# Kernel optimization log

Hardware: AMD Instinct MI355X
Metric: run time of the kernel (lower is better)

The kernel has to match this reference:

```python
import jax, jax.numpy as jnp
import numpy as np

NUM_HEADS = 12
HEAD_DIM = 64
SCALE = HEAD_DIM ** -0.5


def setup_inputs() -> dict:
    key = jax.random.key(0)
    ks = jax.random.split(key, 5)
    B, N, C = 8, 1024, 768
    x = jax.random.normal(ks[0], (B, N, C), dtype=jnp.float32)
    qkv_w = jax.random.normal(ks[1], (3 * C, C), dtype=jnp.float32) * (C ** -0.5)
    qkv_b = jax.random.normal(ks[2], (3 * C,), dtype=jnp.float32) * 0.02
    proj_w = jax.random.normal(ks[3], (C, C), dtype=jnp.float32) * (C ** -0.5)
    proj_b = jax.random.normal(ks[4], (C,), dtype=jnp.float32) * 0.02
    return {"x": x, "qkv_w": qkv_w, "qkv_b": qkv_b, "proj_w": proj_w, "proj_b": proj_b}


def reference(x, qkv_w, qkv_b, proj_w, proj_b):
    B, N, C = x.shape
    H, D = NUM_HEADS, HEAD_DIM
    # qkv projection: (B,N,3C) -> (3,B,H,N,D)
    qkv = (x @ qkv_w.T + qkv_b).reshape(B, N, 3, H, D).transpose(2, 0, 3, 1, 4)
    q, k, v = qkv[0], qkv[1], qkv[2]
    q = q * SCALE
    # full N x N attention scores, softmax over keys
    attn = jax.nn.softmax(jnp.einsum("bhnd,bhmd->bhnm", q, k), axis=-1)
    # Libragrad: detach the softmax map before multiplying with V
    attn = jax.lax.stop_gradient(attn)
    out = jnp.einsum("bhnm,bhmd->bhnd", attn, v)  # (B,H,N,D)
    out = out.transpose(0, 2, 1, 3).reshape(B, N, C)
    return out @ proj_w.T + proj_b
```

## Files before the change

### kernel.cpp

```cpp
#include <hip/hip_runtime.h>

#define NH 12
#define HD 64
#define BB 8
#define SEQ 1024
#define CD 768

typedef __bf16 bf16x8 __attribute__((ext_vector_type(8)));
typedef float f32x4 __attribute__((ext_vector_type(4)));

__device__ __forceinline__ unsigned short f2bf(float f) {
    unsigned int u = __float_as_uint(f);
    u = (u + 0x7fffu + ((u >> 16) & 1u)) >> 16;
    return (unsigned short)u;
}

__device__ __forceinline__ void gld_lds16(const unsigned short* g, unsigned short* l) {
    __builtin_amdgcn_global_load_lds(
        (const __attribute__((address_space(1))) unsigned int*)g,
        (__attribute__((address_space(3))) unsigned int*)l, 16, 0, 0);
}

__device__ __forceinline__ int slot2key(int s) {
    return (s & 3) + 4 * ((s >> 3) & 3) + 16 * ((s >> 2) & 1) + 32 * (s >> 5);
}

#define N4_X 1572864
#define N4_W1 442368
#define N4_W2 147456
__global__ void cast_all(const float* __restrict__ x, const float* __restrict__ w1,
                         const float* __restrict__ w2,
                         unsigned short* __restrict__ ox, unsigned short* __restrict__ ow1,
                         unsigned short* __restrict__ ow2) {
    int i = blockIdx.x * blockDim.x + threadIdx.x;
    const float4* src;
    ushort4* dst;
    if (i < N4_X) {
        src = (const float4*)x + i; dst = (ushort4*)ox + i;
    } else if (i < N4_X + N4_W1) {
        src = (const float4*)w1 + (i - N4_X); dst = (ushort4*)ow1 + (i - N4_X);
    } else if (i < N4_X + N4_W1 + N4_W2) {
        src = (const float4*)w2 + (i - N4_X - N4_W1); dst = (ushort4*)ow2 + (i - N4_X - N4_W1);
    } else return;
    float4 f = *src;
    ushort4 o;
    o.x = f2bf(f.x); o.y = f2bf(f.y); o.z = f2bf(f.z); o.w = f2bf(f.w);
    *dst = o;
}

template<int MODE>
__global__ __launch_bounds__(256)
void gemm_bt(const unsigned short* __restrict__ A, const unsigned short* __restrict__ W,
             const float* __restrict__ bias,
             unsigned short* __restrict__ qb, unsigned short* __restrict__ kb,
             unsigned short* __restrict__ vb, float* __restrict__ fout,
             int M, int N, int K) {
    __shared__ __attribute__((aligned(16))) unsigned short As[2][128 * 32];
    __shared__ __attribute__((aligned(16))) unsigned short Bs[2][128 * 32];

    const int t    = threadIdx.x;
    const int bm0  = blockIdx.x * 128;
    const int bn0  = blockIdx.y * 128;
    const int wave = t >> 6;
    const int lane = t & 63;
    const int wm   = (wave >> 1) * 64;
    const int wn   = (wave & 1) * 64;
    const int col  = lane & 15;
    const int quad = lane >> 4;

    const int srow = t >> 2;
    const int scol = (t & 3) * 8;

    f32x4 acc[4][4];
#pragma unroll
    for (int i = 0; i < 4; i++)
#pragma unroll
        for (int j = 0; j < 4; j++) acc[i][j] = (f32x4){0.f, 0.f, 0.f, 0.f};

    auto stage = [&](int it, unsigned short* Ad, unsigned short* Bd) {
        const int k0 = it << 5;
        gld_lds16(A + (size_t)(bm0 + srow) * K + k0 + scol,      Ad + srow * 32 + scol);
        gld_lds16(A + (size_t)(bm0 + 64 + srow) * K + k0 + scol, Ad + (64 + srow) * 32 + scol);
        gld_lds16(W + (size_t)(bn0 + srow) * K + k0 + scol,      Bd + srow * 32 + scol);
        gld_lds16(W + (size_t)(bn0 + 64 + srow) * K + k0 + scol, Bd + (64 + srow) * 32 + scol);
    };
    auto compute = [&](const unsigned short* Ad, const unsigned short* Bd) {
        bf16x8 af[4], bf[4];
#pragma unroll
        for (int mi = 0; mi < 4; mi++)
            af[mi] = *(const bf16x8*)(Ad + (wm + mi * 16 + col) * 32 + quad * 8);
#pragma unroll
        for (int ni = 0; ni < 4; ni++)
            bf[ni] = *(const bf16x8*)(Bd + (wn + ni * 16 + col) * 32 + quad * 8);
#pragma unroll
        for (int mi = 0; mi < 4; mi++)
#pragma unroll
            for (int ni = 0; ni < 4; ni++)
                acc[mi][ni] = __builtin_amdgcn_mfma_f32_16x16x32_bf16(
                    af[mi], bf[ni], acc[mi][ni], 0, 0, 0);
    };

    const int nIt = K >> 5;
    stage(0, As[0], Bs[0]);
#pragma unroll 1
    for (int it = 0; it < nIt; it += 2) {
        __syncthreads();
        if (it + 1 < nIt) stage(it + 1, As[1], Bs[1]);
        compute(As[0], Bs[0]);
        __syncthreads();
        if (it + 2 < nIt) stage(it + 2, As[0], Bs[0]);
        compute(As[1], Bs[1]);
    }

    if (MODE == 1) {
#pragma unroll
        for (int mi = 0; mi < 4; mi++)
#pragma unroll
            for (int ni = 0; ni < 4; ni++) {
                const int n = bn0 + wn + ni * 16 + col;
                const float bv = bias[n];
#pragma unroll
                for (int r = 0; r < 4; r++) {
                    const int m = bm0 + wm + mi * 16 + quad * 4 + r;
                    fout[(size_t)m * N + n] = acc[mi][ni][r] + bv;
                }
            }
        return;
    }

    const int sel = bn0 / 768;
    const int nb  = bn0 - sel * 768;
    const int b   = bm0 >> 10;
    const int nqb = bm0 & 1023;
    unsigned short* const dstbuf = (sel == 0) ? qb : (sel == 1) ? kb : vb;
    const float scale = (sel == 0) ? 0.18033688f : 1.0f;

#pragma unroll
    for (int ni = 0; ni < 4; ni++) {
        const int hn = nb + wn + ni * 16;
        const int h  = hn >> 6;
        const int d0 = hn & 63;
        const float bv = bias[bn0 + wn + ni * 16 + col];
        unsigned short* const rowbase =
            dstbuf + ((size_t)(b * NH + h) * SEQ) * HD + d0 + col;
#pragma unroll
        for (int mi = 0; mi < 4; mi++)
#pragma unroll
            for (int r = 0; r < 4; r++) {
                const int nq = nqb + wm + mi * 16 + quad * 4 + r;
                rowbase[(size_t)nq * HD] = f2bf((acc[mi][ni][r] + bv) * scale);
            }
    }
}

__global__ __launch_bounds__(256)
void vtrans(const unsigned short* __restrict__ v, unsigned short* __restrict__ vt) {
    __shared__ __attribute__((aligned(16))) unsigned short T[64 * 72];
    const int bh = blockIdx.x;
    const int kt = blockIdx.y;
    const int t  = threadIdx.x;
    const int r  = t >> 2;
    const int c  = (t & 3) * 16;

    const unsigned short* src = v + ((size_t)bh * SEQ + kt * 64 + r) * HD + c;
    *(uint4*)(T + r * 72 + c)     = *(const uint4*)src;
    *(uint4*)(T + r * 72 + c + 8) = *(const uint4*)(src + 8);
    __syncthreads();

    union { unsigned short us[16]; uint4 u4[2]; } o;
#pragma unroll
    for (int j = 0; j < 16; j++) o.us[j] = T[slot2key(c + j) * 72 + r];
    unsigned short* dst = vt + ((size_t)bh * HD + r) * SEQ + kt * 64 + c;
    *(uint4*)dst       = o.u4[0];
    *(uint4*)(dst + 8) = o.u4[1];
}

__global__ __launch_bounds__(256, 4)
void attn_mfma(const unsigned short* __restrict__ qb,
               const unsigned short* __restrict__ kb,
               const unsigned short* __restrict__ vb,
               unsigned short* __restrict__ ob) {
    __shared__ __attribute__((aligned(16))) unsigned short Ks[2][64 * 72];
    __shared__ __attribute__((aligned(16))) unsigned short VT[2][64 * 72];

    const int t  = threadIdx.x;
    const int bh = blockIdx.x;
    const int qt = blockIdx.y;
    const size_t base = (size_t)bh * SEQ * HD;

    const int sr = t >> 2;
    const int sc = (t & 3) * 16;

    const int wave = t >> 6;
    const int lane = t & 63;
    const int col  = lane & 15;
    const int quad = lane >> 4;

    bf16x8 aq0, aq1;
    {
        const int q = qt * 64 + wave * 16 + col;
        aq0 = *(const bf16x8*)(qb + base + (size_t)q * HD + quad * 8);
        aq1 = *(const bf16x8*)(qb + base + (size_t)q * HD + 32 + quad * 8);
    }

    float l_r = 0.f;
    f32x4 accO[4];
#pragma unroll
    for (int di = 0; di < 4; di++) accO[di] = (f32x4){0.f, 0.f, 0.f, 0.f};

    const unsigned short* kp = kb + base + (size_t)sr * HD + sc;
    const unsigned short* vp = vb + base + (size_t)sr * SEQ + sc;
    const int so = sr * 72 + sc;

    uint4 kr0 = *(const uint4*)kp,  kr1 = *(const uint4*)(kp + 8);
    uint4 vr0 = *(const uint4*)vp,  vr1 = *(const uint4*)(vp + 8);
    *(uint4*)(Ks[0] + so)     = kr0;
    *(uint4*)(Ks[0] + so + 8) = kr1;
    *(uint4*)(VT[0] + so)     = vr0;
    *(uint4*)(VT[0] + so + 8) = vr1;
    kr0 = *(const uint4*)(kp + 64 * HD);  kr1 = *(const uint4*)(kp + 64 * HD + 8);
    vr0 = *(const uint4*)(vp + 64);       vr1 = *(const uint4*)(vp + 64 + 8);

    auto chunk = [&](int kc, const unsigned short* Kc, const unsigned short* Vc,
                     unsigned short* Kn, unsigned short* Vn) {
        __syncthreads();
        if (kc < 15) {
            *(uint4*)(Kn + so)     = kr0;
            *(uint4*)(Kn + so + 8) = kr1;
            *(uint4*)(Vn + so)     = vr0;
            *(uint4*)(Vn + so + 8) = vr1;
        }
        if (kc < 14) {
            const unsigned short* kn = kp + (size_t)(kc + 2) * 64 * HD;
            const unsigned short* vn = vp + (size_t)(kc + 2) * 64;
            kr0 = *(const uint4*)kn; kr1 = *(const uint4*)(kn + 8);
            vr0 = *(const uint4*)vn; vr1 = *(const uint4*)(vn + 8);
        }

        f32x4 accT[4];
        __builtin_amdgcn_s_setprio(1);
#pragma unroll
        for (int ni = 0; ni < 4; ni++) {
            bf16x8 bk0 = *(const bf16x8*)(Kc + (ni * 16 + col) * 72 + quad * 8);
            bf16x8 bk1 = *(const bf16x8*)(Kc + (ni * 16 + col) * 72 + 32 + quad * 8);
            f32x4 z = (f32x4){0.f, 0.f, 0.f, 0.f};
            z = __builtin_amdgcn_mfma_f32_16x16x32_bf16(bk0, aq0, z, 0, 0, 0);
            z = __builtin_amdgcn_mfma_f32_16x16x32_bf16(bk1, aq1, z, 0, 0, 0);
            accT[ni] = z;
        }
        __builtin_amdgcn_s_setprio(0);

        union { __bf16 b[16]; bf16x8 v[2]; } apu;
#pragma unroll
        for (int ni = 0; ni < 4; ni++) {
            float p0 = __builtin_exp2f(accT[ni][0]);
            float p1 = __builtin_exp2f(accT[ni][1]);
            float p2 = __builtin_exp2f(accT[ni][2]);
            float p3 = __builtin_exp2f(accT[ni][3]);
            l_r += (p0 + p1) + (p2 + p3);
            apu.b[ni * 4 + 0] = (__bf16)p0;
            apu.b[ni * 4 + 1] = (__bf16)p1;
            apu.b[ni * 4 + 2] = (__bf16)p2;
            apu.b[ni * 4 + 3] = (__bf16)p3;
        }

        __builtin_amdgcn_s_setprio(1);
#pragma unroll
        for (int di = 0; di < 4; di++) {
            bf16x8 bv0 = *(const bf16x8*)(Vc + (di * 16 + col) * 72 + quad * 8);
            bf16x8 bv1 = *(const bf16x8*)(Vc + (di * 16 + col) * 72 + 32 + quad * 8);
            accO[di] = __builtin_amdgcn_mfma_f32_16x16x32_bf16(apu.v[0], bv0, accO[di], 0, 0, 0);
            accO[di] = __builtin_amdgcn_mfma_f32_16x16x32_bf16(apu.v[1], bv1, accO[di], 0, 0, 0);
        }
        __builtin_amdgcn_s_setprio(0);
    };

#pragma unroll 1
    for (int kc2 = 0; kc2 < 16; kc2 += 2) {
        chunk(kc2,     Ks[0], VT[0], Ks[1], VT[1]);
        chunk(kc2 + 1, Ks[1], VT[1], Ks[0], VT[0]);
    }

    const int b = bh / NH, h = bh - b * NH;
    float s = l_r;
    s += __shfl_xor(s, 16);
    s += __shfl_xor(s, 32);
#pragma unroll
    for (int r = 0; r < 4; r++) {
        const float inv = 1.f / __shfl(s, quad * 4 + r);
        const int q = qt * 64 + wave * 16 + quad * 4 + r;
        const size_t rowbase = ((size_t)b * SEQ + q) * CD + h * 64;
#pragma unroll
        for (int di = 0; di < 4; di++)
            ob[rowbase + di * 16 + col] = f2bf(accO[di][r] * inv);
    }
}

extern "C" void kernel_launch(void* const* d_in, const int* in_sizes, int n_in,
                              void* d_out, int out_size, void* d_ws, size_t ws_size,
                              hipStream_t stream) {
    const float* x      = (const float*)d_in[0];
    const float* qkv_w  = (const float*)d_in[1];
    const float* qkv_b  = (const float*)d_in[2];
    const float* proj_w = (const float*)d_in[3];
    const float* proj_b = (const float*)d_in[4];
    float* out = (float*)d_out;

    char* ws = (char*)d_ws;
    unsigned short* x_bf     = (unsigned short*)ws;
    unsigned short* qkvw_bf  = (unsigned short*)(ws + 12582912);
    unsigned short* projw_bf = (unsigned short*)(ws + 12582912 + 3538944);
    unsigned short* q_bf     = (unsigned short*)(ws + 12582912 + 3538944 + 1179648);
    unsigned short* k_bf     = q_bf + 6291456;
    unsigned short* v_bf     = k_bf + 6291456;
    unsigned short* vt_bf    = x_bf;
    unsigned short* attn_bf  = v_bf;

    cast_all<<<8448, 256, 0, stream>>>(x, qkv_w, proj_w, x_bf, qkvw_bf, projw_bf);

    gemm_bt<0><<<dim3(64, 18), 256, 0, stream>>>(x_bf, qkvw_bf, qkv_b,
                                                 q_bf, k_bf, v_bf, nullptr,
                                                 8192, 2304, 768);

    vtrans<<<dim3(96, 16), 256, 0, stream>>>(v_bf, vt_bf);

    attn_mfma<<<dim3(96, 16), 256, 0, stream>>>(q_bf, k_bf, vt_bf, attn_bf);

    gemm_bt<1><<<dim3(64, 6), 256, 0, stream>>>(attn_bf, projw_bf, proj_b,
                                                nullptr, nullptr, nullptr, out,
                                                8192, 768, 768);
}
```

Baseline: 198.4 us.

## Fuse fp32-to-bf16 cast of x into QKV GEMM A-tile loading

The separate pass that cast x to bf16 is removed. The QKV GEMM now loads fp32 A tiles into registers two iterations ahead, converts them to bf16 and writes them to LDS after each compute step. This drops a full write and re-read of the bf16 copy of x and shrinks the cast kernel to weights only. In exchange the GEMM reads twice as many bytes for A, uses more registers for prefetch, and A loads no longer go directly to LDS, which may hurt occupancy or overlap. Rounding now comes from the compiler's __bf16 conversion instead of the manual routine.

```diff
diff --git a/kernel.cpp b/kernel.cpp
--- a/kernel.cpp
+++ b/kernel.cpp
@@ -25,22 +25,17 @@
     return (s & 3) + 4 * ((s >> 3) & 3) + 16 * ((s >> 2) & 1) + 32 * (s >> 5);
 }
 
-#define N4_X 1572864
 #define N4_W1 442368
 #define N4_W2 147456
-__global__ void cast_all(const float* __restrict__ x, const float* __restrict__ w1,
-                         const float* __restrict__ w2,
-                         unsigned short* __restrict__ ox, unsigned short* __restrict__ ow1,
-                         unsigned short* __restrict__ ow2) {
+__global__ void cast_all(const float* __restrict__ w1, const float* __restrict__ w2,
+                         unsigned short* __restrict__ ow1, unsigned short* __restrict__ ow2) {
     int i = blockIdx.x * blockDim.x + threadIdx.x;
     const float4* src;
     ushort4* dst;
-    if (i < N4_X) {
-        src = (const float4*)x + i; dst = (ushort4*)ox + i;
-    } else if (i < N4_X + N4_W1) {
-        src = (const float4*)w1 + (i - N4_X); dst = (ushort4*)ow1 + (i - N4_X);
-    } else if (i < N4_X + N4_W1 + N4_W2) {
-        src = (const float4*)w2 + (i - N4_X - N4_W1); dst = (ushort4*)ow2 + (i - N4_X - N4_W1);
+    if (i < N4_W1) {
+        src = (const float4*)w1 + i; dst = (ushort4*)ow1 + i;
+    } else if (i < N4_W1 + N4_W2) {
+        src = (const float4*)w2 + (i - N4_W1); dst = (ushort4*)ow2 + (i - N4_W1);
     } else return;
     float4 f = *src;
     ushort4 o;
@@ -50,7 +45,8 @@
 
 template<int MODE>
 __global__ __launch_bounds__(256)
-void gemm_bt(const unsigned short* __restrict__ A, const unsigned short* __restrict__ W,
+void gemm_bt(const float* __restrict__ Af, const unsigned short* __restrict__ Ab,
+             const unsigned short* __restrict__ W,
              const float* __restrict__ bias,
              unsigned short* __restrict__ qb, unsigned short* __restrict__ kb,
              unsigned short* __restrict__ vb, float* __restrict__ fout,
@@ -77,12 +73,35 @@
 #pragma unroll
         for (int j = 0; j < 4; j++) acc[i][j] = (f32x4){0.f, 0.f, 0.f, 0.f};
 
-    auto stage = [&](int it, unsigned short* Ad, unsigned short* Bd) {
+    auto stageB = [&](int it, unsigned short* Bd) {
         const int k0 = it << 5;
-        gld_lds16(A + (size_t)(bm0 + srow) * K + k0 + scol,      Ad + srow * 32 + scol);
-        gld_lds16(A + (size_t)(bm0 + 64 + srow) * K + k0 + scol, Ad + (64 + srow) * 32 + scol);
         gld_lds16(W + (size_t)(bn0 + srow) * K + k0 + scol,      Bd + srow * 32 + scol);
         gld_lds16(W + (size_t)(bn0 + 64 + srow) * K + k0 + scol, Bd + (64 + srow) * 32 + scol);
+    };
+    auto stageAb = [&](int it, unsigned short* Ad) {
+        const int k0 = it << 5;
+        gld_lds16(Ab + (size_t)(bm0 + srow) * K + k0 + scol,      Ad + srow * 32 + scol);
+        gld_lds16(Ab + (size_t)(bm0 + 64 + srow) * K + k0 + scol, Ad + (64 + srow) * 32 + scol);
+    };
+    auto loadA = [&](int it, float4 (&r)[4]) {
+        const int k0 = it << 5;
+        const float* p0 = Af + (size_t)(bm0 + srow) * K + k0 + scol;
+        const float* p1 = Af + (size_t)(bm0 + 64 + srow) * K + k0 + scol;
+        r[0] = *(const float4*)p0; r[1] = *(const float4*)(p0 + 4);
+        r[2] = *(const float4*)p1; r[3] = *(const float4*)(p1 + 4);
+    };
+    auto writeA = [&](const float4 (&r)[4], unsigned short* Ad) {
+        union { __bf16 b[8]; uint4 u; } w0, w1;
+        w0.b[0] = (__bf16)r[0].x; w0.b[1] = (__bf16)r[0].y;
+        w0.b[2] = (__bf16)r[0].z; w0.b[3] = (__bf16)r[0].w;
+        w0.b[4] = (__bf16)r[1].x; w0.b[5] = (__bf16)r[1].y;
+        w0.b[6] = (__bf16)r[1].z; w0.b[7] = (__bf16)r[1].w;
+        w1.b[0] = (__bf16)r[2].x; w1.b[1] = (__bf16)r[2].y;
+        w1.b[2] = (__bf16)r[2].z; w1.b[3] = (__bf16)r[2].w;
+        w1.b[4] = (__bf16)r[3].x; w1.b[5] = (__bf16)r[3].y;
+        w1.b[6] = (__bf16)r[3].z; w1.b[7] = (__bf16)r[3].w;
+        *(uint4*)(Ad + srow * 32 + scol)        = w0.u;
+        *(uint4*)(Ad + (64 + srow) * 32 + scol) = w1.u;
     };
     auto compute = [&](const unsigned short* Ad, const unsigned short* Bd) {
         bf16x8 af[4], bf[4];
@@ -101,15 +120,39 @@
     };
 
     const int nIt = K >> 5;
-    stage(0, As[0], Bs[0]);
+    float4 ra0[4], ra1[4];
+    if constexpr (MODE == 0) {
+        loadA(0, ra0); writeA(ra0, As[0]);
+        loadA(1, ra1);
+        stageB(0, Bs[0]);
+    } else {
+        stageAb(0, As[0]);
+        stageB(0, Bs[0]);
+    }
 #pragma unroll 1
     for (int it = 0; it < nIt; it += 2) {
         __syncthreads();
-        if (it + 1 < nIt) stage(it + 1, As[1], Bs[1]);
+        if (it + 1 < nIt) stageB(it + 1, Bs[1]);
+        if constexpr (MODE == 0) {
+            if (it + 2 < nIt) loadA(it + 2, ra0);
+        } else {
+            if (it + 1 < nIt) stageAb(it + 1, As[1]);
+        }
         compute(As[0], Bs[0]);
+        if constexpr (MODE == 0) {
+            if (it + 1 < nIt) writeA(ra1, As[1]);
+        }
         __syncthreads();
-        if (it + 2 < nIt) stage(it + 2, As[0], Bs[0]);
+        if (it + 2 < nIt) stageB(it + 2, Bs[0]);
+        if constexpr (MODE == 0) {
+            if (it + 3 < nIt) loadA(it + 3, ra1);
+        } else {
+            if (it + 2 < nIt) stageAb(it + 2, As[0]);
+        }
         compute(As[1], Bs[1]);
+        if constexpr (MODE == 0) {
+            if (it + 2 < nIt) writeA(ra0, As[0]);
+        }
     }
 
     if (MODE == 1) {
@@ -316,9 +359,9 @@
     unsigned short* vt_bf    = x_bf;
     unsigned short* attn_bf  = v_bf;
 
-    cast_all<<<8448, 256, 0, stream>>>(x, qkv_w, proj_w, x_bf, qkvw_bf, projw_bf);
-
-    gemm_bt<0><<<dim3(64, 18), 256, 0, stream>>>(x_bf, qkvw_bf, qkv_b,
+    cast_all<<<2304, 256, 0, stream>>>(qkv_w, proj_w, qkvw_bf, projw_bf);
+
+    gemm_bt<0><<<dim3(64, 18), 256, 0, stream>>>(x, nullptr, qkvw_bf, qkv_b,
                                                  q_bf, k_bf, v_bf, nullptr,
                                                  8192, 2304, 768);
 
@@ -326,7 +369,7 @@
 
     attn_mfma<<<dim3(96, 16), 256, 0, stream>>>(q_bf, k_bf, vt_bf, attn_bf);
 
-    gemm_bt<1><<<dim3(64, 6), 256, 0, stream>>>(attn_bf, projw_bf, proj_b,
+    gemm_bt<1><<<dim3(64, 6), 256, 0, stream>>>(nullptr, attn_bf, projw_bf, proj_b,
                                                 nullptr, nullptr, nullptr, out,
                                                 8192, 768, 768);
 }
```

Measured after the change: 217.4 us. 1.1x slower.

## Process two query sub-tiles per wave to reuse K/V tiles in attention

Applied to the files above, without the earlier changes.

Each wave now handles 32 query rows (two 16-row sub-tiles) instead of 16, so each block covers 128 queries and the grid's query dimension halves. Every K and V fragment read from LDS feeds twice as many MFMAs, and K/V global traffic per query is halved. The cost is more live registers (two sets of accumulators and Q fragments), so launch bounds drop from 4 to 3 blocks per SM. The grid also shrinks to 768 blocks, which lowers parallelism.

```diff
diff --git a/kernel.cpp b/kernel.cpp
--- a/kernel.cpp
+++ b/kernel.cpp
@@ -175,7 +175,7 @@
     *(uint4*)(dst + 8) = o.u4[1];
 }
 
-__global__ __launch_bounds__(256, 4)
+__global__ __launch_bounds__(256, 3)
 void attn_mfma(const unsigned short* __restrict__ qb,
                const unsigned short* __restrict__ kb,
                const unsigned short* __restrict__ vb,
@@ -196,17 +196,20 @@
     const int col  = lane & 15;
     const int quad = lane >> 4;
 
-    bf16x8 aq0, aq1;
-    {
-        const int q = qt * 64 + wave * 16 + col;
-        aq0 = *(const bf16x8*)(qb + base + (size_t)q * HD + quad * 8);
-        aq1 = *(const bf16x8*)(qb + base + (size_t)q * HD + 32 + quad * 8);
-    }
-
-    float l_r = 0.f;
-    f32x4 accO[4];
-#pragma unroll
-    for (int di = 0; di < 4; di++) accO[di] = (f32x4){0.f, 0.f, 0.f, 0.f};
+    bf16x8 aq[2][2];
+#pragma unroll
+    for (int u = 0; u < 2; u++) {
+        const int q = qt * 128 + (2 * wave + u) * 16 + col;
+        aq[u][0] = *(const bf16x8*)(qb + base + (size_t)q * HD + quad * 8);
+        aq[u][1] = *(const bf16x8*)(qb + base + (size_t)q * HD + 32 + quad * 8);
+    }
+
+    float l_r[2] = {0.f, 0.f};
+    f32x4 accO[2][4];
+#pragma unroll
+    for (int u = 0; u < 2; u++)
+#pragma unroll
+        for (int di = 0; di < 4; di++) accO[u][di] = (f32x4){0.f, 0.f, 0.f, 0.f};
 
     const unsigned short* kp = kb + base + (size_t)sr * HD + sc;
     const unsigned short* vp = vb + base + (size_t)sr * SEQ + sc;
@@ -237,40 +240,48 @@
             vr0 = *(const uint4*)vn; vr1 = *(const uint4*)(vn + 8);
         }
 
-        f32x4 accT[4];
+        f32x4 accT[2][4];
         __builtin_amdgcn_s_setprio(1);
 #pragma unroll
         for (int ni = 0; ni < 4; ni++) {
             bf16x8 bk0 = *(const bf16x8*)(Kc + (ni * 16 + col) * 72 + quad * 8);
             bf16x8 bk1 = *(const bf16x8*)(Kc + (ni * 16 + col) * 72 + 32 + quad * 8);
-            f32x4 z = (f32x4){0.f, 0.f, 0.f, 0.f};
-            z = __builtin_amdgcn_mfma_f32_16x16x32_bf16(bk0, aq0, z, 0, 0, 0);
-            z = __builtin_amdgcn_mfma_f32_16x16x32_bf16(bk1, aq1, z, 0, 0, 0);
-            accT[ni] = z;
+#pragma unroll
+            for (int u = 0; u < 2; u++) {
+                f32x4 z = (f32x4){0.f, 0.f, 0.f, 0.f};
+                z = __builtin_amdgcn_mfma_f32_16x16x32_bf16(bk0, aq[u][0], z, 0, 0, 0);
+                z = __builtin_amdgcn_mfma_f32_16x16x32_bf16(bk1, aq[u][1], z, 0, 0, 0);
+                accT[u][ni] = z;
+            }
         }
         __builtin_amdgcn_s_setprio(0);
 
-        union { __bf16 b[16]; bf16x8 v[2]; } apu;
-#pragma unroll
-        for (int ni = 0; ni < 4; ni++) {
-            float p0 = __builtin_exp2f(accT[ni][0]);
-            float p1 = __builtin_exp2f(accT[ni][1]);
-            float p2 = __builtin_exp2f(accT[ni][2]);
-            float p3 = __builtin_exp2f(accT[ni][3]);
-            l_r += (p0 + p1) + (p2 + p3);
-            apu.b[ni * 4 + 0] = (__bf16)p0;
-            apu.b[ni * 4 + 1] = (__bf16)p1;
-            apu.b[ni * 4 + 2] = (__bf16)p2;
-            apu.b[ni * 4 + 3] = (__bf16)p3;
-        }
+        union { __bf16 b[16]; bf16x8 v[2]; } apu[2];
+#pragma unroll
+        for (int u = 0; u < 2; u++)
+#pragma unroll
+            for (int ni = 0; ni < 4; ni++) {
+                float p0 = __builtin_exp2f(accT[u][ni][0]);
+                float p1 = __builtin_exp2f(accT[u][ni][1]);
+                float p2 = __builtin_exp2f(accT[u][ni][2]);
+                float p3 = __builtin_exp2f(accT[u][ni][3]);
+                l_r[u] += (p0 + p1) + (p2 + p3);
+                apu[u].b[ni * 4 + 0] = (__bf16)p0;
+                apu[u].b[ni * 4 + 1] = (__bf16)p1;
+                apu[u].b[ni * 4 + 2] = (__bf16)p2;
+                apu[u].b[ni * 4 + 3] = (__bf16)p3;
+            }
 
         __builtin_amdgcn_s_setprio(1);
 #pragma unroll
         for (int di = 0; di < 4; di++) {
             bf16x8 bv0 = *(const bf16x8*)(Vc + (di * 16 + col) * 72 + quad * 8);
             bf16x8 bv1 = *(const bf16x8*)(Vc + (di * 16 + col) * 72 + 32 + quad * 8);
-            accO[di] = __builtin_amdgcn_mfma_f32_16x16x32_bf16(apu.v[0], bv0, accO[di], 0, 0, 0);
-            accO[di] = __builtin_amdgcn_mfma_f32_16x16x32_bf16(apu.v[1], bv1, accO[di], 0, 0, 0);
+#pragma unroll
+            for (int u = 0; u < 2; u++) {
+                accO[u][di] = __builtin_amdgcn_mfma_f32_16x16x32_bf16(apu[u].v[0], bv0, accO[u][di], 0, 0, 0);
+                accO[u][di] = __builtin_amdgcn_mfma_f32_16x16x32_bf16(apu[u].v[1], bv1, accO[u][di], 0, 0, 0);
+            }
         }
         __builtin_amdgcn_s_setprio(0);
     };
@@ -282,17 +293,20 @@
     }
 
     const int b = bh / NH, h = bh - b * NH;
-    float s = l_r;
-    s += __shfl_xor(s, 16);
-    s += __shfl_xor(s, 32);
-#pragma unroll
-    for (int r = 0; r < 4; r++) {
-        const float inv = 1.f / __shfl(s, quad * 4 + r);
-        const int q = qt * 64 + wave * 16 + quad * 4 + r;
-        const size_t rowbase = ((size_t)b * SEQ + q) * CD + h * 64;
-#pragma unroll
-        for (int di = 0; di < 4; di++)
-            ob[rowbase + di * 16 + col] = f2bf(accO[di][r] * inv);
+#pragma unroll
+    for (int u = 0; u < 2; u++) {
+        float s = l_r[u];
+        s += __shfl_xor(s, 16);
+        s += __shfl_xor(s, 32);
+#pragma unroll
+        for (int r = 0; r < 4; r++) {
+            const float inv = 1.f / __shfl(s, quad * 4 + r);
+            const int q = qt * 128 + (2 * wave + u) * 16 + quad * 4 + r;
+            const size_t rowbase = ((size_t)b * SEQ + q) * CD + h * 64;
+#pragma unroll
+            for (int di = 0; di < 4; di++)
+                ob[rowbase + di * 16 + col] = f2bf(accO[u][di][r] * inv);
+        }
     }
 }
 
@@ -324,7 +338,7 @@
 
     vtrans<<<dim3(96, 16), 256, 0, stream>>>(v_bf, vt_bf);
 
-    attn_mfma<<<dim3(96, 16), 256, 0, stream>>>(q_bf, k_bf, vt_bf, attn_bf);
+    attn_mfma<<<dim3(96, 8), 256, 0, stream>>>(q_bf, k_bf, vt_bf, attn_bf);
 
     gemm_bt<1><<<dim3(64, 6), 256, 0, stream>>>(attn_bf, projw_bf, proj_b,
                                                 nullptr, nullptr, nullptr, out,
```

Measured after the change: 195.7 us. About the same (-1.4%).
